# Optimization experiments

Measured on AMD Instinct MI355X. Metric: run time of the kernel, lower is better.

Reference implementation:

```python
import jax, jax.numpy as jnp
import numpy as np

GRID_H = 64
GRID_W = 64


def make_grid(h, w):
    # torch.meshgrid([arange(h), arange(w)], indexing='xy') -> shape (w, h);
    # grid[i, j] = (j + 0.5, i + 0.5). With h == w == 64 this is square.
    gx, gy = jnp.meshgrid(jnp.arange(h, dtype=jnp.float32),
                          jnp.arange(w, dtype=jnp.float32), indexing='xy')
    return jnp.stack([gx, gy], axis=-1) + 0.5  # (w, h, 2)


def setup_inputs() -> dict:
    key = jax.random.key(0)
    k1, k2 = jax.random.split(key)
    x = jax.random.normal(k1, (4, 128, 64, 64), dtype=jnp.float32)
    y = jax.random.normal(k2, (4, 128, 64, 64), dtype=jnp.float32)
    return {"x": x, "y": y}


def reference(x, y):
    b, c, hx, wx = x.shape
    _, _, hy, wy = y.shape
    scale = c ** (-0.5)
    grids = make_grid(GRID_H, GRID_W)[:hy, :wy].reshape(-1, 2)  # (hy*wy, 2)

    x_ = x.reshape(b, c, hx * wx)
    y_ = y.reshape(b, c, hy * wy)
    # (b, q, k) attention over all key pixels
    attn = jax.nn.softmax(jnp.einsum('bcq,bck->bqk', x_, y_) * scale, axis=-1)
    uv = jnp.einsum('bqk,kt->bqt', attn, grids)  # (b, hx*wx, 2)
    uv = uv.reshape(b, hx, wx, 2)
    # normalize to [-1, 1]
    norm = jnp.asarray([wy, hy], dtype=uv.dtype)
    uv = uv / norm * 2.0 - 1.0
    return uv
```

## Files before the change

kernel.cpp:

```cpp
#include <hip/hip_runtime.h>
#include <math.h>

typedef __attribute__((ext_vector_type(8))) _Float16 f16x8;
typedef __attribute__((ext_vector_type(16))) float f32x16;

#define NPIX 4096
#define C_DIM 128
#define SCALE 0.08838834764831845f

#define WS_NEED ((size_t)4 << 20)

__global__ __launch_bounds__(256) void conv_y(const float* __restrict__ y,
                                              char* __restrict__ ws)
{
    __shared__ float T[32][132];
    const int wg  = blockIdx.x;
    const int xcd = wg & 7;
    const int b   = xcd >> 1;
    const int sl  = ((xcd & 1) << 6) | (wg >> 3);
    const int k0  = sl * 32;
    const int t   = threadIdx.x;

    {
        const int c = t >> 1, half = t & 1;
        const float* srow = y + ((size_t)b * C_DIM + c) * NPIX + k0 + half * 16;
        float4 rv[4];
        #pragma unroll
        for (int u = 0; u < 4; ++u) rv[u] = *(const float4*)(srow + u * 4);
        #pragma unroll
        for (int u = 0; u < 4; ++u) {
            T[half * 16 + u * 4 + 0][c] = rv[u].x;
            T[half * 16 + u * 4 + 1][c] = rv[u].y;
            T[half * 16 + u * 4 + 2][c] = rv[u].z;
            T[half * 16 + u * 4 + 3][c] = rv[u].w;
        }
    }
    __syncthreads();

    char* panel = ws + (size_t)b * (NPIX * 256);
    const int k = t >> 3, g2 = t & 7;
    f16x8 v0, v1;
    #pragma unroll
    for (int m = 0; m < 8; ++m) {
        v0[m] = (_Float16)T[k][g2 * 16 + m];
        v1[m] = (_Float16)T[k][g2 * 16 + 8 + m];
    }
    const int key = k0 + k, s = key & 7;
    char* drow = panel + (size_t)key * 256;
    *(f16x8*)(drow + (((2 * g2)     ^ s) << 4)) = v0;
    *(f16x8*)(drow + (((2 * g2 + 1) ^ s) << 4)) = v1;
}

__global__ __launch_bounds__(256, 2) void uv_main(const char* __restrict__ ws,
                                                  const float* __restrict__ x,
                                                  float* __restrict__ out)
{
    __shared__ __align__(16) char Ys[2][32768];

    const int t = threadIdx.x, w = t >> 6, l = t & 63;
    const int l32 = l & 31, h32 = l >> 5;
    const int wg  = blockIdx.x;
    const int xcd = wg & 7;
    const int b   = xcd >> 1;
    const int qt  = ((xcd & 1) << 6) | (wg >> 3);
    const int q0  = qt * 32;

    f16x8 bh[8], bl[8];
    {
        const float* xq = x + (size_t)b * C_DIM * NPIX + q0 + l32;
        #pragma unroll
        for (int c = 0; c < 8; ++c) {
            f16x8 hh, ll;
            #pragma unroll
            for (int j = 0; j < 8; ++j) {
                const float f = xq[(size_t)(c * 16 + h32 * 8 + j) * NPIX] * SCALE;
                const _Float16 fh = (_Float16)f;
                hh[j] = fh;
                ll[j] = (_Float16)(f - (float)fh);
            }
            bh[c] = hh;
            bl[c] = ll;
        }
    }

    const char* panel = ws + (size_t)b * (NPIX * 256);

    const int arow = w * 32 + l32;
    int aoff[8];
    #pragma unroll
    for (int c = 0; c < 8; ++c)
        aoff[c] = arow * 256 + (((c * 2 + h32) ^ (arow & 7)) << 4);

    int soff[8];
    #pragma unroll
    for (int i = 0; i < 8; ++i) soff[i] = (w * 32 + i * 4) * 256 + l * 16;

    #pragma unroll
    for (int i = 0; i < 8; ++i)
        __builtin_amdgcn_global_load_lds(
            (const __attribute__((address_space(1))) void*)(panel + soff[i]),
            (__attribute__((address_space(3))) void*)(&Ys[0][soff[i]]), 16, 0, 0);

    const float tadd = (float)((w & 1) * 32 + 4 * h32) + 0.5f;
    const float gyw  = (float)(w >> 1) + 0.5f;
    float den = 0.f, nu = 0.f, nv = 0.f;

    for (int kt = 0; kt < 32; ++kt) {
        char* cur = Ys[kt & 1];

        __builtin_amdgcn_s_waitcnt(0x0F70 );

        if (kt < 31) {
            const char* gt = panel + (size_t)(kt + 1) * 32768;
            char* nb = Ys[(kt & 1) ^ 1];
            #pragma unroll
            for (int i = 0; i < 8; ++i)
                __builtin_amdgcn_global_load_lds(
                    (const __attribute__((address_space(1))) void*)(gt + soff[i]),
                    (__attribute__((address_space(3))) void*)(&nb[soff[i]]), 16, 0, 0);
        }

        f32x16 acc = {0.f, 0.f, 0.f, 0.f, 0.f, 0.f, 0.f, 0.f,
                      0.f, 0.f, 0.f, 0.f, 0.f, 0.f, 0.f, 0.f};
        #pragma unroll
        for (int c = 0; c < 8; ++c) {
            const f16x8 A = *(const f16x8*)(cur + aoff[c]);
            acc = __builtin_amdgcn_mfma_f32_32x32x16_f16(A, bh[c], acc, 0, 0, 0);
            acc = __builtin_amdgcn_mfma_f32_32x32x16_f16(A, bl[c], acc, 0, 0, 0);
        }

        float ps = 0.f, pc = 0.f;
        #pragma unroll
        for (int r = 0; r < 16; ++r) {
            const float p = __expf(acc[r]);
            ps += p;
            pc += p * (float)((r & 3) + 8 * (r >> 2));
        }
        den += ps;
        nu  += pc + tadd * ps;
        nv  += (2.0f * (float)kt + gyw) * ps;
    }

    den += __shfl_xor(den, 32);
    nu  += __shfl_xor(nu,  32);
    nv  += __shfl_xor(nv,  32);

    __syncthreads();
    float* red = (float*)&Ys[0][0];
    if (h32 == 0) {
        const int base = (w * 32 + l32) * 3;
        red[base + 0] = den;
        red[base + 1] = nu;
        red[base + 2] = nv;
    }
    __syncthreads();
    if (t < 32) {
        float d = 0.f, u = 0.f, v = 0.f;
        #pragma unroll
        for (int ww = 0; ww < 4; ++ww) {
            d += red[(ww * 32 + t) * 3 + 0];
            u += red[(ww * 32 + t) * 3 + 1];
            v += red[(ww * 32 + t) * 3 + 2];
        }
        const float inv = 1.0f / d;
        *(float2*)(out + ((size_t)b * NPIX + q0 + t) * 2) =
            make_float2(u * inv * 0.03125f - 1.0f, v * inv * 0.03125f - 1.0f);
    }
}

__global__ __launch_bounds__(256, 2) void uv_attn_kernel(
    const float* __restrict__ x, const float* __restrict__ y, float* __restrict__ out)
{
    __shared__ float Xs[C_DIM][32];
    __shared__ float Ysf[64][128];
    const int tid = threadIdx.x;
    const int wgid = blockIdx.x;
    const int xcd = wgid & 7;
    const int b = xcd & 3;
    const int q0 = (((xcd >> 2) << 6) | (wgid >> 3)) * 32;
    const float* xb = x + (size_t)b * C_DIM * NPIX + q0;
    {
        const int cr = tid >> 3;
        const int cc = (tid & 7) << 2;
        #pragma unroll
        for (int i = 0; i < 4; ++i) {
            float4 v = *(const float4*)(xb + (size_t)(cr + (i << 5)) * NPIX + cc);
            v.x *= SCALE; v.y *= SCALE; v.z *= SCALE; v.w *= SCALE;
            *(float4*)(&Xs[cr + (i << 5)][cc]) = v;
        }
    }
    const int rg = tid >> 4;
    const int lane16 = tid & 15;
    const int r0 = rg << 1;
    const int col0 = lane16 << 3;
    float gxv[8];
    #pragma unroll
    for (int j2 = 0; j2 < 8; ++j2) gxv[j2] = (float)((col0 & 63) + j2) + 0.5f;
    const float gyb = (float)(lane16 >> 3) + 0.5f;
    float m_run[2] = {-INFINITY, -INFINITY};
    float den[2] = {0.f, 0.f}, nu[2] = {0.f, 0.f}, nv[2] = {0.f, 0.f};
    const int yr = tid >> 5;
    const int yc = (tid & 31) << 2;
    const float* ybase = y + (size_t)b * C_DIM * NPIX;
    for (int kt = 0; kt < 32; ++kt) {
        float S[2][8];
        #pragma unroll
        for (int r = 0; r < 2; ++r)
            #pragma unroll
            for (int j2 = 0; j2 < 8; ++j2) S[r][j2] = 0.f;
        #pragma unroll
        for (int cb = 0; cb < 2; ++cb) {
            __syncthreads();
            const float* yt = ybase + (size_t)(cb << 6) * NPIX + kt * 128;
            #pragma unroll
            for (int i = 0; i < 8; ++i)
                *(float4*)(&Ysf[yr + (i << 3)][yc]) =
                    *(const float4*)(yt + (size_t)(yr + (i << 3)) * NPIX + yc);
            __syncthreads();
            const int cbase = cb << 6;
            #pragma unroll 16
            for (int c = 0; c < 64; ++c) {
                const float2 xa = *(const float2*)(&Xs[cbase + c][r0]);
                const float4 ya = *(const float4*)(&Ysf[c][col0]);
                const float4 yb4 = *(const float4*)(&Ysf[c][col0 + 4]);
                S[0][0] += xa.x * ya.x;  S[0][1] += xa.x * ya.y;
                S[0][2] += xa.x * ya.z;  S[0][3] += xa.x * ya.w;
                S[0][4] += xa.x * yb4.x; S[0][5] += xa.x * yb4.y;
                S[0][6] += xa.x * yb4.z; S[0][7] += xa.x * yb4.w;
                S[1][0] += xa.y * ya.x;  S[1][1] += xa.y * ya.y;
                S[1][2] += xa.y * ya.z;  S[1][3] += xa.y * ya.w;
                S[1][4] += xa.y * yb4.x; S[1][5] += xa.y * yb4.y;
                S[1][6] += xa.y * yb4.z; S[1][7] += xa.y * yb4.w;
            }
        }
        const float gy = gyb + 2.0f * (float)kt;
        #pragma unroll
        for (int r = 0; r < 2; ++r) {
            float tmax = S[r][0];
            #pragma unroll
            for (int j2 = 1; j2 < 8; ++j2) tmax = fmaxf(tmax, S[r][j2]);
            #pragma unroll
            for (int mk = 8; mk >= 1; mk >>= 1) tmax = fmaxf(tmax, __shfl_xor(tmax, mk, 16));
            const float mnew = fmaxf(m_run[r], tmax);
            const float alpha = __expf(m_run[r] - mnew);
            m_run[r] = mnew;
            float psum = 0.f, pu = 0.f;
            #pragma unroll
            for (int j2 = 0; j2 < 8; ++j2) {
                const float p = __expf(S[r][j2] - mnew);
                psum += p; pu += p * gxv[j2];
            }
            den[r] = den[r] * alpha + psum;
            nu[r] = nu[r] * alpha + pu;
            nv[r] = nv[r] * alpha + gy * psum;
        }
    }
    #pragma unroll
    for (int r = 0; r < 2; ++r)
        #pragma unroll
        for (int mk = 8; mk >= 1; mk >>= 1) {
            den[r] += __shfl_xor(den[r], mk, 16);
            nu[r] += __shfl_xor(nu[r], mk, 16);
            nv[r] += __shfl_xor(nv[r], mk, 16);
        }
    if (lane16 == 0) {
        #pragma unroll
        for (int r = 0; r < 2; ++r) {
            const float inv = 1.0f / den[r];
            const int q = q0 + r0 + r;
            *(float2*)(out + ((size_t)b * NPIX + q) * 2) =
                make_float2(nu[r] * inv * 0.03125f - 1.0f, nv[r] * inv * 0.03125f - 1.0f);
        }
    }
}

extern "C" void kernel_launch(void* const* d_in, const int* in_sizes, int n_in,
                              void* d_out, int out_size, void* d_ws, size_t ws_size,
                              hipStream_t stream) {
    const float* x = (const float*)d_in[0];
    const float* y = (const float*)d_in[1];
    float* out = (float*)d_out;
    if (ws_size >= WS_NEED) {
        hipLaunchKernelGGL(conv_y, dim3(512), dim3(256), 0, stream, y, (char*)d_ws);
        hipLaunchKernelGGL(uv_main, dim3(512), dim3(256), 0, stream,
                           (const char*)d_ws, x, out);
    } else {
        hipLaunchKernelGGL(uv_attn_kernel, dim3(512), dim3(256), 0, stream, x, y, out);
    }
}
```

Before: 107.1 us.

## Switch uv_main to 16x16x32 MFMA, drop hi/lo split, 64-query tiles

Restructures the main attention kernel. It now uses 16x16x32 f16 MFMA with 8 waves per 512-thread block, and each block handles 64 queries instead of 32, so every loaded key tile is reused across more queries. The split of x into high and low f16 parts is removed, which halves the number of MFMAs but reduces the precision of the query operand to plain f16. Per-lane softmax accumulation and the cross-lane reduction are reworked to match the new output layout.

```diff
diff --git a/kernel.cpp b/kernel.cpp
--- a/kernel.cpp
+++ b/kernel.cpp
@@ -2,7 +2,7 @@
 #include <math.h>
 
 typedef __attribute__((ext_vector_type(8))) _Float16 f16x8;
-typedef __attribute__((ext_vector_type(16))) float f32x16;
+typedef __attribute__((ext_vector_type(4))) float f32x4;
 
 #define NPIX 4096
 #define C_DIM 128
@@ -51,59 +51,56 @@
     *(f16x8*)(drow + (((2 * g2 + 1) ^ s) << 4)) = v1;
 }
 
-__global__ __launch_bounds__(256, 2) void uv_main(const char* __restrict__ ws,
+__global__ __launch_bounds__(512, 2) void uv_main(const char* __restrict__ ws,
                                                   const float* __restrict__ x,
                                                   float* __restrict__ out)
 {
     __shared__ __align__(16) char Ys[2][32768];
 
     const int t = threadIdx.x, w = t >> 6, l = t & 63;
-    const int l32 = l & 31, h32 = l >> 5;
+    const int n16 = l & 15, quad = l >> 4;
     const int wg  = blockIdx.x;
     const int xcd = wg & 7;
     const int b   = xcd >> 1;
-    const int qt  = ((xcd & 1) << 6) | (wg >> 3);
-    const int q0  = qt * 32;
-
-    f16x8 bh[8], bl[8];
+    const int qt  = ((xcd & 1) << 5) | (wg >> 3);
+    const int q0  = qt * 64;
+
+    f16x8 bx[4][4];
     {
-        const float* xq = x + (size_t)b * C_DIM * NPIX + q0 + l32;
-        #pragma unroll
-        for (int c = 0; c < 8; ++c) {
-            f16x8 hh, ll;
-            #pragma unroll
-            for (int j = 0; j < 8; ++j) {
-                const float f = xq[(size_t)(c * 16 + h32 * 8 + j) * NPIX] * SCALE;
-                const _Float16 fh = (_Float16)f;
-                hh[j] = fh;
-                ll[j] = (_Float16)(f - (float)fh);
+        const float* xq = x + (size_t)b * C_DIM * NPIX + q0 + n16;
+        #pragma unroll
+        for (int cc = 0; cc < 4; ++cc)
+            #pragma unroll
+            for (int qg = 0; qg < 4; ++qg) {
+                f16x8 hh;
+                #pragma unroll
+                for (int j = 0; j < 8; ++j)
+                    hh[j] = (_Float16)(xq[(size_t)(cc * 32 + quad * 8 + j) * NPIX + qg * 16] * SCALE);
+                bx[cc][qg] = hh;
             }
-            bh[c] = hh;
-            bl[c] = ll;
-        }
     }
 
     const char* panel = ws + (size_t)b * (NPIX * 256);
 
-    const int arow = w * 32 + l32;
-    int aoff[8];
-    #pragma unroll
-    for (int c = 0; c < 8; ++c)
-        aoff[c] = arow * 256 + (((c * 2 + h32) ^ (arow & 7)) << 4);
-
-    int soff[8];
-    #pragma unroll
-    for (int i = 0; i < 8; ++i) soff[i] = (w * 32 + i * 4) * 256 + l * 16;
-
-    #pragma unroll
-    for (int i = 0; i < 8; ++i)
+    const int arow = w * 16 + n16;
+    int aoff[4];
+    #pragma unroll
+    for (int cc = 0; cc < 4; ++cc)
+        aoff[cc] = arow * 256 + (((cc * 4 + quad) ^ (n16 & 7)) << 4);
+
+    int soff[4];
+    #pragma unroll
+    for (int i = 0; i < 4; ++i) soff[i] = (w * 16 + i * 4) * 256 + l * 16;
+
+    #pragma unroll
+    for (int i = 0; i < 4; ++i)
         __builtin_amdgcn_global_load_lds(
             (const __attribute__((address_space(1))) void*)(panel + soff[i]),
             (__attribute__((address_space(3))) void*)(&Ys[0][soff[i]]), 16, 0, 0);
 
-    const float tadd = (float)((w & 1) * 32 + 4 * h32) + 0.5f;
-    const float gyw  = (float)(w >> 1) + 0.5f;
-    float den = 0.f, nu = 0.f, nv = 0.f;
+    const float gxb = (float)((w & 3) * 16 + quad * 4) + 0.5f;
+    const float gyw = (float)(w >> 2) + 0.5f;
+    float den[4] = {0.f, 0.f, 0.f, 0.f}, nu[4] = {0.f, 0.f, 0.f, 0.f}, nv[4] = {0.f, 0.f, 0.f, 0.f};
 
     for (int kt = 0; kt < 32; ++kt) {
         char* cur = Ys[kt & 1];
@@ -114,53 +111,68 @@
             const char* gt = panel + (size_t)(kt + 1) * 32768;
             char* nb = Ys[(kt & 1) ^ 1];
             #pragma unroll
-            for (int i = 0; i < 8; ++i)
+            for (int i = 0; i < 4; ++i)
                 __builtin_amdgcn_global_load_lds(
                     (const __attribute__((address_space(1))) void*)(gt + soff[i]),
                     (__attribute__((address_space(3))) void*)(&nb[soff[i]]), 16, 0, 0);
         }
 
-        f32x16 acc = {0.f, 0.f, 0.f, 0.f, 0.f, 0.f, 0.f, 0.f,
-                      0.f, 0.f, 0.f, 0.f, 0.f, 0.f, 0.f, 0.f};
-        #pragma unroll
-        for (int c = 0; c < 8; ++c) {
-            const f16x8 A = *(const f16x8*)(cur + aoff[c]);
-            acc = __builtin_amdgcn_mfma_f32_32x32x16_f16(A, bh[c], acc, 0, 0, 0);
-            acc = __builtin_amdgcn_mfma_f32_32x32x16_f16(A, bl[c], acc, 0, 0, 0);
-        }
-
-        float ps = 0.f, pc = 0.f;
-        #pragma unroll
-        for (int r = 0; r < 16; ++r) {
-            const float p = __expf(acc[r]);
-            ps += p;
-            pc += p * (float)((r & 3) + 8 * (r >> 2));
-        }
-        den += ps;
-        nu  += pc + tadd * ps;
-        nv  += (2.0f * (float)kt + gyw) * ps;
-    }
-
-    den += __shfl_xor(den, 32);
-    nu  += __shfl_xor(nu,  32);
-    nv  += __shfl_xor(nv,  32);
-
+        f32x4 acc[4];
+        #pragma unroll
+        for (int qg = 0; qg < 4; ++qg) acc[qg] = (f32x4){0.f, 0.f, 0.f, 0.f};
+
+        #pragma unroll
+        for (int cc = 0; cc < 4; ++cc) {
+            const f16x8 A = *(const f16x8*)(cur + aoff[cc]);
+            #pragma unroll
+            for (int qg = 0; qg < 4; ++qg)
+                acc[qg] = __builtin_amdgcn_mfma_f32_16x16x32_f16(A, bx[cc][qg], acc[qg], 0, 0, 0);
+        }
+
+        const float gy = 2.0f * (float)kt + gyw;
+        #pragma unroll
+        for (int qg = 0; qg < 4; ++qg) {
+            float ps = 0.f, pc = 0.f;
+            #pragma unroll
+            for (int r = 0; r < 4; ++r) {
+                const float p = __expf(acc[qg][r]);
+                ps += p;
+                pc += p * (float)r;
+            }
+            den[qg] += ps;
+            nu[qg]  += pc + gxb * ps;
+            nv[qg]  += gy * ps;
+        }
+    }
+
+    #pragma unroll
+    for (int qg = 0; qg < 4; ++qg) {
+        #pragma unroll
+        for (int mk = 16; mk <= 32; mk <<= 1) {
+            den[qg] += __shfl_xor(den[qg], mk);
+            nu[qg]  += __shfl_xor(nu[qg],  mk);
+            nv[qg]  += __shfl_xor(nv[qg],  mk);
+        }
+    }
     __syncthreads();
     float* red = (float*)&Ys[0][0];
-    if (h32 == 0) {
-        const int base = (w * 32 + l32) * 3;
-        red[base + 0] = den;
-        red[base + 1] = nu;
-        red[base + 2] = nv;
+    if (quad == 0) {
+        #pragma unroll
+        for (int qg = 0; qg < 4; ++qg) {
+            const int base = (w * 64 + qg * 16 + n16) * 3;
+            red[base + 0] = den[qg];
+            red[base + 1] = nu[qg];
+            red[base + 2] = nv[qg];
+        }
     }
     __syncthreads();
-    if (t < 32) {
+    if (t < 64) {
         float d = 0.f, u = 0.f, v = 0.f;
         #pragma unroll
-        for (int ww = 0; ww < 4; ++ww) {
-            d += red[(ww * 32 + t) * 3 + 0];
-            u += red[(ww * 32 + t) * 3 + 1];
-            v += red[(ww * 32 + t) * 3 + 2];
+        for (int ww = 0; ww < 8; ++ww) {
+            d += red[(ww * 64 + t) * 3 + 0];
+            u += red[(ww * 64 + t) * 3 + 1];
+            v += red[(ww * 64 + t) * 3 + 2];
         }
         const float inv = 1.0f / d;
         *(float2*)(out + ((size_t)b * NPIX + q0 + t) * 2) =
@@ -282,7 +294,7 @@
     float* out = (float*)d_out;
     if (ws_size >= WS_NEED) {
         hipLaunchKernelGGL(conv_y, dim3(512), dim3(256), 0, stream, y, (char*)d_ws);
-        hipLaunchKernelGGL(uv_main, dim3(512), dim3(256), 0, stream,
+        hipLaunchKernelGGL(uv_main, dim3(256), dim3(512), 0, stream,
                            (const char*)d_ws, x, out);
     } else {
         hipLaunchKernelGGL(uv_attn_kernel, dim3(512), dim3(256), 0, stream, x, y, out);
```

New measurement: 92.47 us. -13.7%, faster.
